# Kernel tuning notes

Hardware: AMD Instinct MI355X
Metric: run time of the kernel (lower is better)

The kernel has to match this reference:

```python
import jax, jax.numpy as jnp
import numpy as np

B, T, C = 2, 2048, 1024
NH, NKV, HD = 16, 4, 64   # n_head, n_kv_head, head_dim
WIN_LEFT = 1024           # flash-attn window_size=(1024, 0), causal


def rmsnorm(x):
    # F.rms_norm with no weight: x / sqrt(mean(x^2) + eps), eps = dtype eps
    eps = jnp.finfo(x.dtype).eps
    return x * jax.lax.rsqrt(jnp.mean(x * x, axis=-1, keepdims=True) + eps)


def rope(x, cos, sin):
    # x: [B,T,H,D]; cos/sin: [T,1,D/2] broadcast over batch and heads
    d = x.shape[-1] // 2
    x1, x2 = x[..., :d], x[..., d:]
    return jnp.concatenate([x1 * cos + x2 * sin, -x1 * sin + x2 * cos], axis=-1)


def setup_inputs() -> dict:
    key = jax.random.key(0)
    ks = jax.random.split(key, 9)
    return {
        "x":  jax.random.normal(ks[0], (B, T, C), jnp.float32),
        "x0": jax.random.normal(ks[1], (B, T, C), jnp.float32),
        "ve": jax.random.normal(ks[2], (B, T, NKV, HD), jnp.float32),
        "cos": jax.random.normal(ks[3], (T, 1, HD // 2), jnp.float32),
        "sin": jax.random.normal(ks[4], (T, 1, HD // 2), jnp.float32),
        "Wq": jax.random.normal(ks[5], (NH * HD, C), jnp.float32) * 0.02,
        "Wk": jax.random.normal(ks[6], (NKV * HD, C), jnp.float32) * 0.02,
        "Wv": jax.random.normal(ks[7], (NKV * HD, C), jnp.float32) * 0.02,
        "Wo": jax.random.normal(ks[8], (C, C), jnp.float32) * 0.02,
    }


def reference(x, x0, ve, cos, sin, Wq, Wk, Wv, Wo):
    b, t, c = x.shape
    q = (x @ Wq.T).reshape(b, t, NH, HD)
    k = (x @ Wk.T).reshape(b, t, NKV, HD)
    v = (x @ Wv.T).reshape(b, t, NKV, HD)
    v_init = v
    # is_late branch: halve_value, add_init_qkv, add_init_v all active
    v = 0.5 * v
    x0n = rmsnorm(x0)
    q = 0.5 * q + 0.5 * (x0n @ Wq.T).reshape(b, t, NH, HD)
    k = 0.5 * k + 0.5 * (x0n @ Wk.T).reshape(b, t, NKV, HD)
    v = v + 0.5 * (x0n @ Wv.T).reshape(b, t, NKV, HD)
    v = v + 0.5 * ve
    # rotary -> rms-norm -> scale 1.2 on q and k
    q = rmsnorm(rope(q, cos, sin)) * 1.2
    k = rmsnorm(rope(k, cos, sin)) * 1.2
    # GQA: repeat kv heads to match query heads
    g = NH // NKV
    k = jnp.repeat(k, g, axis=2)
    v = jnp.repeat(v, g, axis=2)
    scores = jnp.einsum("bqhd,bkhd->bhqk", q, k) / np.float32(np.sqrt(HD))
    i = jnp.arange(t)[:, None]
    j = jnp.arange(t)[None, :]
    mask = (j <= i) & (i - j <= WIN_LEFT)  # causal sliding window
    scores = jnp.where(mask, scores, jnp.finfo(scores.dtype).min)
    att = jax.nn.softmax(scores, axis=-1)
    y = jnp.einsum("bhqk,bkhd->bqhd", att, v).reshape(b, t, c)
    y = y @ Wo.T
    return (y, v_init)
```

## Files before the change

### kernel.cpp

```cpp
#include <hip/hip_runtime.h>


typedef __attribute__((ext_vector_type(8))) short bf16x8;
typedef __attribute__((ext_vector_type(4))) float f32x4;
typedef __attribute__((ext_vector_type(16))) float f32x16;
typedef unsigned short u16;
typedef unsigned int u32;

#define B_ 2
#define T_ 2048
#define C_ 1024
#define NH_ 16
#define NKV_ 4
#define WIN_ 1024
#define M_ (B_*T_)
#define EPS_ 1.1920929e-07f

__device__ __forceinline__ u16 f2bf(float f) {
  u32 u = __float_as_uint(f);
  u32 r = (u + 0x7fffu + ((u >> 16) & 1u)) >> 16;
  return (u16)r;
}
__device__ __forceinline__ float bf2f(u16 h) { return __uint_as_float(((u32)h) << 16); }

__device__ __forceinline__ void gload16(const u16* g, u16* l) {
  __builtin_amdgcn_global_load_lds((const __attribute__((address_space(1))) u32*)g,
                                   (__attribute__((address_space(3))) u32*)l, 16, 0, 0);
}
#define SWZ(row, kg) ((((row)) << 7) + ((((kg) ^ ((row) & 7))) << 4))
#define SWO(lane) (8 * (((lane) & 7) ^ (((lane) >> 3) & 7)))

__global__ __launch_bounds__(256) void k_convert_all(const float* __restrict__ Wq,
                                                     const float* __restrict__ Wk,
                                                     const float* __restrict__ Wv,
                                                     const float* __restrict__ Wo,
                                                     u16* __restrict__ dst) {
  int i4 = blockIdx.x * 256 + threadIdx.x;
  const float* src; int s0;
  if (i4 < 262144)      { src = Wq; s0 = 0; }
  else if (i4 < 327680) { src = Wk; s0 = 262144; }
  else if (i4 < 393216) { src = Wv; s0 = 327680; }
  else                  { src = Wo; s0 = 393216; }
  float4 v = ((const float4*)src)[i4 - s0];
  ushort4 o;
  o.x = f2bf(v.x); o.y = f2bf(v.y); o.z = f2bf(v.z); o.w = f2bf(v.w);
  ((ushort4*)dst)[i4] = o;
}

__global__ __launch_bounds__(256) void k_rms_combine(const float* __restrict__ x,
                                                     const float* __restrict__ x0,
                                                     u16* __restrict__ xbf,
                                                     u16* __restrict__ xmbf) {
  int row = blockIdx.x;
  int tid = threadIdx.x, lane = tid & 63, w = tid >> 6;
  const float4* px0 = (const float4*)(x0 + (size_t)row * C_);
  const float4* px  = (const float4*)(x  + (size_t)row * C_);
  float4 v0 = px0[tid];
  float ss = v0.x * v0.x + v0.y * v0.y + v0.z * v0.z + v0.w * v0.w;
  #pragma unroll
  for (int m = 1; m < 64; m <<= 1) ss += __shfl_xor(ss, m, 64);
  __shared__ float red[4];
  if (lane == 0) red[w] = ss;
  __syncthreads();
  float tot = red[0] + red[1] + red[2] + red[3];
  float rn = rsqrtf(tot * (1.0f / C_) + EPS_);
  float4 vx = px[tid];
  ushort4 om, ox;
  om.x = f2bf(0.5f * (vx.x + v0.x * rn));
  om.y = f2bf(0.5f * (vx.y + v0.y * rn));
  om.z = f2bf(0.5f * (vx.z + v0.z * rn));
  om.w = f2bf(0.5f * (vx.w + v0.w * rn));
  ox.x = f2bf(vx.x); ox.y = f2bf(vx.y); ox.z = f2bf(vx.z); ox.w = f2bf(vx.w);
  ((ushort4*)(xmbf + (size_t)row * C_))[tid] = om;
  ((ushort4*)(xbf  + (size_t)row * C_))[tid] = ox;
}

__device__ __forceinline__ void gemm_core(const u16* pa0, const u16* pb0,
                                          u16* Asl, u16* Bsl,
                                          int lane, int w, int r0, int c0,
                                          f32x4 acc[4][2]) {
  #pragma unroll
  for (int c = 0; c < 4; c++) gload16(pa0 + (size_t)c * 32 * 1024, Asl + (c * 32 + w * 8) * 64);
  #pragma unroll
  for (int c = 0; c < 2; c++) gload16(pb0 + (size_t)c * 32 * 1024, Bsl + (c * 32 + w * 8) * 64);
  int cur = 0;
  for (int kt = 0; kt < 1024; kt += 64) {
    __syncthreads();
    if (kt + 64 < 1024) {
      int nxt = cur ^ 1;
      #pragma unroll
      for (int c = 0; c < 4; c++)
        gload16(pa0 + (size_t)c * 32 * 1024 + kt + 64, Asl + nxt * 8192 + (c * 32 + w * 8) * 64);
      #pragma unroll
      for (int c = 0; c < 2; c++)
        gload16(pb0 + (size_t)c * 32 * 1024 + kt + 64, Bsl + nxt * 4096 + (c * 32 + w * 8) * 64);
    }
    const char* Ab = (const char*)(Asl + cur * 8192);
    const char* Bb = (const char*)(Bsl + cur * 4096);
    bf16x8 af[2][4], bfr[2][2];
    #pragma unroll
    for (int ks = 0; ks < 2; ks++) {
      #pragma unroll
      for (int fi = 0; fi < 4; fi++)
        af[ks][fi] = *(const bf16x8*)(Ab + SWZ(r0 + fi * 16 + (lane & 15), ks * 4 + (lane >> 4)));
      #pragma unroll
      for (int fj = 0; fj < 2; fj++)
        bfr[ks][fj] = *(const bf16x8*)(Bb + SWZ(c0 + fj * 16 + (lane & 15), ks * 4 + (lane >> 4)));
    }
    #pragma unroll
    for (int ks = 0; ks < 2; ks++)
      #pragma unroll
      for (int fi = 0; fi < 4; fi++)
        #pragma unroll
        for (int fj = 0; fj < 2; fj++)
          acc[fi][fj] = __builtin_amdgcn_mfma_f32_16x16x32_bf16(af[ks][fi], bfr[ks][fj], acc[fi][fj], 0, 0, 0);
    cur ^= 1;
  }
}

__global__ __launch_bounds__(256) void k_gemm_qkv(const u16* __restrict__ xm,
                                                  const u16* __restrict__ xb,
                                                  const u16* __restrict__ Wq,
                                                  const u16* __restrict__ Wk,
                                                  const u16* __restrict__ Wv,
                                                  u16* __restrict__ qpre,
                                                  u16* __restrict__ kpre,
                                                  u16* __restrict__ vmid,
                                                  float* __restrict__ vinit) {
  __shared__ u16 Asl[2 * 8192];
  __shared__ u16 Bsl[2 * 4096];
  int tid = threadIdx.x, lane = tid & 63, w = tid >> 6;
  int m0 = blockIdx.x * 128, bn = blockIdx.y, n0 = bn * 64;
  const u16* A; const u16* Wseg; int nseg;
  if (bn < 16)      { A = xm; Wseg = Wq; nseg = n0; }
  else if (bn < 20) { A = xm; Wseg = Wk; nseg = n0 - 1024; }
  else if (bn < 24) { A = xm; Wseg = Wv; nseg = n0 - 1280; }
  else              { A = xb; Wseg = Wv; nseg = n0 - 1536; }
  int swo = SWO(lane);
  const u16* pa0 = A    + (size_t)(m0 + w * 8 + (lane >> 3)) * 1024 + swo;
  const u16* pb0 = Wseg + (size_t)(nseg + w * 8 + (lane >> 3)) * 1024 + swo;
  int r0 = (w >> 1) * 64, c0 = (w & 1) * 32;
  f32x4 acc[4][2] = {};
  gemm_core(pa0, pb0, Asl, Bsl, lane, w, r0, c0, acc);
  #pragma unroll
  for (int fi = 0; fi < 4; fi++)
    #pragma unroll
    for (int fj = 0; fj < 2; fj++)
      #pragma unroll
      for (int i = 0; i < 4; i++) {
        int m = m0 + r0 + fi * 16 + (lane >> 4) * 4 + i;
        int nl = nseg + c0 + fj * 16 + (lane & 15);
        float v = acc[fi][fj][i];
        if (bn < 16)      qpre[(size_t)m * 1024 + nl] = f2bf(v);
        else if (bn < 20) kpre[(size_t)m * 256 + nl] = f2bf(v);
        else if (bn < 24) vmid[(size_t)m * 256 + nl] = f2bf(v);
        else              vinit[(size_t)m * 256 + nl] = v;
      }
}

__global__ __launch_bounds__(256) void k_gemm_o(const u16* __restrict__ A,
                                                const u16* __restrict__ W,
                                                float* __restrict__ y) {
  __shared__ u16 Asl[2 * 8192];
  __shared__ u16 Bsl[2 * 4096];
  int tid = threadIdx.x, lane = tid & 63, w = tid >> 6;
  int m0 = blockIdx.x * 128, n0 = blockIdx.y * 64;
  int swo = SWO(lane);
  const u16* pa0 = A + (size_t)(m0 + w * 8 + (lane >> 3)) * 1024 + swo;
  const u16* pb0 = W + (size_t)(n0 + w * 8 + (lane >> 3)) * 1024 + swo;
  int r0 = (w >> 1) * 64, c0 = (w & 1) * 32;
  f32x4 acc[4][2] = {};
  gemm_core(pa0, pb0, Asl, Bsl, lane, w, r0, c0, acc);
  #pragma unroll
  for (int fi = 0; fi < 4; fi++)
    #pragma unroll
    for (int fj = 0; fj < 2; fj++)
      #pragma unroll
      for (int i = 0; i < 4; i++) {
        int m = m0 + r0 + fi * 16 + (lane >> 4) * 4 + i;
        int n = n0 + c0 + fj * 16 + (lane & 15);
        y[(size_t)m * 1024 + n] = acc[fi][fj][i];
      }
}

__global__ __launch_bounds__(256) void k_qk_post(const u16* __restrict__ qpre,
                                                 const u16* __restrict__ kpre,
                                                 const float* __restrict__ cosp,
                                                 const float* __restrict__ sinp,
                                                 u16* __restrict__ Qh,
                                                 u16* __restrict__ Kh) {
  int w = threadIdx.x >> 6, lane = threadIdx.x & 63;
  int vid = blockIdx.x * 4 + w;
  const int NQ = B_ * T_ * NH_;
  int t; float val; size_t dst; u16* out; float scale;
  if (vid < NQ) {
    int h = vid & 15; t = (vid >> 4) & 2047; int b = vid >> 15;
    val = bf2f(qpre[(size_t)vid * 64 + lane]);
    dst = (((size_t)(b * NH_ + h) * T_) + t) * 64 + lane;
    out = Qh; scale = 0.15f;
  } else {
    int kid = vid - NQ;
    int hk = kid & 3; t = (kid >> 2) & 2047; int b = kid >> 13;
    val = bf2f(kpre[(size_t)kid * 64 + lane]);
    dst = (((size_t)(b * NKV_ + hk) * T_) + t) * 64 + lane;
    out = Kh; scale = 1.2f;
  }
  int di = lane & 31;
  float partner = __shfl_xor(val, 32, 64);
  float c = cosp[t * 32 + di], s = sinp[t * 32 + di];
  float r = (lane < 32) ? (val * c + partner * s) : (val * c - partner * s);
  float ss = r * r;
  #pragma unroll
  for (int m2 = 1; m2 < 64; m2 <<= 1) ss += __shfl_xor(ss, m2, 64);
  r *= rsqrtf(ss * (1.0f / 64.0f) + EPS_) * scale;
  out[dst] = f2bf(r);
}

__global__ __launch_bounds__(256) void k_vt(const u16* __restrict__ vmid,
                                            const float* __restrict__ ve,
                                            u16* __restrict__ VtG) {
  __shared__ u16 S[64][72];
  int tid = threadIdx.x;
  int t0 = blockIdx.x * 64, hk = blockIdx.y, b = blockIdx.z;
  {
    int tl = tid >> 2, dg = (tid & 3) * 16;
    const int4* pvm = (const int4*)(vmid + (size_t)(b * T_ + t0 + tl) * 256 + hk * 64 + dg);
    const float4* pve = (const float4*)(ve + ((size_t)(b * T_ + t0 + tl) * 4 + hk) * 64 + dg);
    int4 vv[2]; vv[0] = pvm[0]; vv[1] = pvm[1];
    const u16* vm = (const u16*)vv;
    float4 vf[4]; vf[0] = pve[0]; vf[1] = pve[1]; vf[2] = pve[2]; vf[3] = pve[3];
    const float* vfp = (const float*)vf;
    u16 r[16];
    #pragma unroll
    for (int e = 0; e < 16; e++) r[e] = f2bf(bf2f(vm[e]) + 0.5f * vfp[e]);
    *(int4*)&S[tl][dg] = *(int4*)&r[0];
    *(int4*)&S[tl][dg + 8] = *(int4*)&r[8];
  }
  __syncthreads();
  {
    int dl = tid >> 2, tg = (tid & 3) * 16;
    u16 r[16];
    #pragma unroll
    for (int j = 0; j < 16; j++) r[j] = S[tg + j][dl];
    u16* o = VtG + ((size_t)((b * NKV_ + hk) * 64 + dl)) * T_ + t0 + tg;
    *(int4*)&o[0] = *(int4*)&r[0];
    *(int4*)&o[8] = *(int4*)&r[8];
  }
}

__global__ __launch_bounds__(512) void k_attn(const u16* __restrict__ Qh,
                                              const u16* __restrict__ Kh,
                                              const u16* __restrict__ VtG,
                                              u16* __restrict__ ao) {
  __shared__ u16 Ksl[2][64 * 64];
  __shared__ u16 Vsl[2][64 * 64];
  __shared__ float Sc[8][32];
  int tid = threadIdx.x, lane = tid & 63, w = tid >> 6;
  int hi = lane >> 5, qc = lane & 31;
  int qt = blockIdx.x, h = blockIdx.y, b = blockIdx.z;
  int hk = h >> 2;
  int q0 = qt * 256, wq0 = q0 + w * 32;
  const u16* Qp = Qh + ((size_t)(b * NH_ + h) * T_) * 64;
  const u16* Kp = Kh + ((size_t)(b * NKV_ + hk) * T_) * 64;
  int swo = SWO(lane);
  const u16* pk0 = Kp + (size_t)(w * 8 + (lane >> 3)) * 64 + swo;
  const u16* pv0 = VtG + ((size_t)((b * NKV_ + hk) * 64 + w * 8 + (lane >> 3))) * T_ + swo;

  bf16x8 qf[4];
  #pragma unroll
  for (int ds = 0; ds < 4; ds++)
    qf[ds] = *(const bf16x8*)(Qp + (size_t)(wq0 + qc) * 64 + ds * 16 + hi * 8);

  f32x16 o0 = {}, o1 = {};
  float mrun = -1e4f, lrun = 0.f;
  int kt_lo = q0 - WIN_; if (kt_lo < 0) kt_lo = 0;
  int kt_hi = q0 + 192;

  gload16(pk0 + (size_t)kt_lo * 64, &Ksl[0][w * 512]);
  gload16(pv0 + kt_lo,              &Vsl[0][w * 512]);
  int cur = 0;
  for (int kt = kt_lo; kt <= kt_hi; kt += 64) {
    __syncthreads();
    if (kt + 64 <= kt_hi) {
      gload16(pk0 + (size_t)(kt + 64) * 64, &Ksl[cur ^ 1][w * 512]);
      gload16(pv0 + kt + 64,                &Vsl[cur ^ 1][w * 512]);
    }
    if (kt <= wq0 + 31 && kt + 63 >= wq0 - WIN_) {
      const char* Kb = (const char*)&Ksl[cur][0];
      const char* Vb = (const char*)&Vsl[cur][0];
      f32x16 st[2] = {};
      #pragma unroll
      for (int kt2 = 0; kt2 < 2; kt2++)
        #pragma unroll
        for (int ds = 0; ds < 4; ds++) {
          bf16x8 kf = *(const bf16x8*)(Kb + SWZ(kt2 * 32 + qc, 2 * ds + hi));
          st[kt2] = __builtin_amdgcn_mfma_f32_32x32x16_bf16(kf, qf[ds], st[kt2], 0, 0, 0);
        }
      bool full = (kt + 63 <= wq0) && (wq0 + 31 - kt <= WIN_);
      int D0 = wq0 + qc - kt;
      float p[2][16];
      float tmax = -1e30f;
      #pragma unroll
      for (int kt2 = 0; kt2 < 2; kt2++)
        #pragma unroll
        for (int r = 0; r < 16; r++) {
          float sv = st[kt2][r];
          if (!full) {
            int jl = 32 * kt2 + (r & 3) + 8 * (r >> 2) + 4 * hi;
            sv = (jl <= D0 && jl >= D0 - WIN_) ? sv : -1e9f;
          }
          p[kt2][r] = sv;
          tmax = fmaxf(tmax, sv);
        }
      tmax = fmaxf(tmax, __shfl_xor(tmax, 32, 64));
      if (__any(tmax > mrun + 8.0f)) {
        float mnew = fmaxf(mrun, tmax);
        float alpha = __expf(mrun - mnew);
        mrun = mnew; lrun *= alpha;
        if (hi == 0) Sc[w][qc] = alpha;
        #pragma unroll
        for (int r = 0; r < 16; r++) {
          float al = Sc[w][(r & 3) + 8 * (r >> 2) + 4 * hi];
          o0[r] *= al; o1[r] *= al;
        }
      }
      float rsum = 0.f;
      u32 pw[2][8];
      #pragma unroll
      for (int kt2 = 0; kt2 < 2; kt2++)
        #pragma unroll
        for (int c = 0; c < 8; c++) {
          float pe = __expf(p[kt2][2 * c] - mrun);
          float po = __expf(p[kt2][2 * c + 1] - mrun);
          rsum += pe + po;
          pw[kt2][c] = __builtin_amdgcn_perm(__float_as_uint(po), __float_as_uint(pe), 0x07060302u);
        }
      rsum += __shfl_xor(rsum, 32, 64);
      lrun += rsum;
      #pragma unroll
      for (int kt2 = 0; kt2 < 2; kt2++)
        #pragma unroll
        for (int ksp = 0; ksp < 2; ksp++) {
          union { u32 uw[4]; bf16x8 v; } U;
          #pragma unroll
          for (int c = 0; c < 2; c++) {
            u32 x = pw[kt2][4 * ksp + c];
            u32 y = pw[kt2][4 * ksp + 2 + c];
            u32 xs = (u32)__shfl_xor((int)x, 32, 64);
            u32 ys = (u32)__shfl_xor((int)y, 32, 64);
            U.uw[c]     = hi ? ys : x;
            U.uw[2 + c] = hi ? y : xs;
          }
          int ks = 2 * kt2 + ksp;
          bf16x8 v0 = *(const bf16x8*)(Vb + SWZ(qc,      2 * ks + hi));
          bf16x8 v1 = *(const bf16x8*)(Vb + SWZ(32 + qc, 2 * ks + hi));
          o0 = __builtin_amdgcn_mfma_f32_32x32x16_bf16(U.v, v0, o0, 0, 0, 0);
          o1 = __builtin_amdgcn_mfma_f32_32x32x16_bf16(U.v, v1, o1, 0, 0, 0);
        }
    }
    cur ^= 1;
  }
  if (hi == 0) Sc[w][qc] = 1.0f / lrun;
  #pragma unroll
  for (int r = 0; r < 16; r++) {
    int q = (r & 3) + 8 * (r >> 2) + 4 * hi;
    float il = Sc[w][q];
    size_t base = ((size_t)(b * T_ + wq0 + q) * NH_ + h) * 64;
    ao[base + qc]      = f2bf(o0[r] * il);
    ao[base + 32 + qc] = f2bf(o1[r] * il);
  }
}

extern "C" void kernel_launch(void* const* d_in, const int* in_sizes, int n_in,
                              void* d_out, int out_size, void* d_ws, size_t ws_size,
                              hipStream_t stream) {
  const float* x    = (const float*)d_in[0];
  const float* x0   = (const float*)d_in[1];
  const float* ve   = (const float*)d_in[2];
  const float* cosp = (const float*)d_in[3];
  const float* sinp = (const float*)d_in[4];
  const float* Wq   = (const float*)d_in[5];
  const float* Wk   = (const float*)d_in[6];
  const float* Wv   = (const float*)d_in[7];
  const float* Wo   = (const float*)d_in[8];
  float* out = (float*)d_out;

  u16* ws = (u16*)d_ws;
  size_t off = 0;
  u16* xbf  = ws + off; off += (size_t)M_ * C_;
  u16* xmbf = ws + off; off += (size_t)M_ * C_;
  u16* Wqb  = ws + off; off += (size_t)1024 * 1024;
  u16* Wkb  = ws + off; off += (size_t)256 * 1024;
  u16* Wvb  = ws + off; off += (size_t)256 * 1024;
  u16* Wob  = ws + off; off += (size_t)1024 * 1024;
  u16* qpre = ws + off; off += (size_t)M_ * 1024;
  u16* kpre = ws + off; off += (size_t)M_ * 256;
  u16* vmid = ws + off; off += (size_t)M_ * 256;
  u16* VtG  = ws + off; off += (size_t)B_ * NKV_ * 64 * T_;
  u16* aob = xbf;
  u16* Qhb = xmbf;
  u16* Khb = Wqb;

  k_convert_all<<<2560, 256, 0, stream>>>(Wq, Wk, Wv, Wo, Wqb);
  k_rms_combine<<<4096, 256, 0, stream>>>(x, x0, xbf, xmbf);
  k_gemm_qkv<<<dim3(32, 28), 256, 0, stream>>>(xmbf, xbf, Wqb, Wkb, Wvb,
                                               qpre, kpre, vmid, out + (size_t)M_ * C_);
  k_qk_post<<<20480, 256, 0, stream>>>(qpre, kpre, cosp, sinp, Qhb, Khb);
  k_vt<<<dim3(32, 4, 2), 256, 0, stream>>>(vmid, ve, VtG);
  k_attn<<<dim3(8, 16, 2), 512, 0, stream>>>(Qhb, Khb, VtG, aob);
  k_gemm_o<<<dim3(32, 16), 256, 0, stream>>>(aob, Wob, out);
}
```

Measured before the change: 214.2 us.

## Rewrite attention as split-KV two-wave blocks and enlarge GEMM tiles to 128x128

The attention kernel now gives each 128-thread block one 32-query tile and splits the key range between two waves. Each wave streams K/V fragments straight from global memory into registers instead of staging them in shared memory, and the two partial softmax states are merged at the end through shared memory. Blocks are ordered with the heaviest query tiles first and grouped by KV head for cache reuse. The GEMMs switch to 128x128 tiles with 4x4 MFMA accumulators per wave, but drop the double-buffered LDS prefetch for a single buffer with two barriers per k-step. This trades load latency hiding for more reuse per tile.

```diff
diff --git a/kernel.cpp b/kernel.cpp
--- a/kernel.cpp
+++ b/kernel.cpp
@@ -78,43 +78,32 @@
 __device__ __forceinline__ void gemm_core(const u16* pa0, const u16* pb0,
                                           u16* Asl, u16* Bsl,
                                           int lane, int w, int r0, int c0,
-                                          f32x4 acc[4][2]) {
-  #pragma unroll
-  for (int c = 0; c < 4; c++) gload16(pa0 + (size_t)c * 32 * 1024, Asl + (c * 32 + w * 8) * 64);
-  #pragma unroll
-  for (int c = 0; c < 2; c++) gload16(pb0 + (size_t)c * 32 * 1024, Bsl + (c * 32 + w * 8) * 64);
-  int cur = 0;
+                                          f32x4 acc[4][4]) {
+  const char* Ab = (const char*)Asl;
+  const char* Bb = (const char*)Bsl;
   for (int kt = 0; kt < 1024; kt += 64) {
     __syncthreads();
-    if (kt + 64 < 1024) {
-      int nxt = cur ^ 1;
-      #pragma unroll
-      for (int c = 0; c < 4; c++)
-        gload16(pa0 + (size_t)c * 32 * 1024 + kt + 64, Asl + nxt * 8192 + (c * 32 + w * 8) * 64);
-      #pragma unroll
-      for (int c = 0; c < 2; c++)
-        gload16(pb0 + (size_t)c * 32 * 1024 + kt + 64, Bsl + nxt * 4096 + (c * 32 + w * 8) * 64);
-    }
-    const char* Ab = (const char*)(Asl + cur * 8192);
-    const char* Bb = (const char*)(Bsl + cur * 4096);
-    bf16x8 af[2][4], bfr[2][2];
-    #pragma unroll
-    for (int ks = 0; ks < 2; ks++) {
-      #pragma unroll
-      for (int fi = 0; fi < 4; fi++)
-        af[ks][fi] = *(const bf16x8*)(Ab + SWZ(r0 + fi * 16 + (lane & 15), ks * 4 + (lane >> 4)));
-      #pragma unroll
-      for (int fj = 0; fj < 2; fj++)
-        bfr[ks][fj] = *(const bf16x8*)(Bb + SWZ(c0 + fj * 16 + (lane & 15), ks * 4 + (lane >> 4)));
-    }
+    #pragma unroll
+    for (int c = 0; c < 4; c++) {
+      gload16(pa0 + (size_t)c * 32 * 1024 + kt, Asl + (c * 32 + w * 8) * 64);
+      gload16(pb0 + (size_t)c * 32 * 1024 + kt, Bsl + (c * 32 + w * 8) * 64);
+    }
+    __syncthreads();
+    bf16x8 af[2][4], bfr[2][4];
+    #pragma unroll
+    for (int ks = 0; ks < 2; ks++)
+      #pragma unroll
+      for (int fi = 0; fi < 4; fi++) {
+        af[ks][fi]  = *(const bf16x8*)(Ab + SWZ(r0 + fi * 16 + (lane & 15), ks * 4 + (lane >> 4)));
+        bfr[ks][fi] = *(const bf16x8*)(Bb + SWZ(c0 + fi * 16 + (lane & 15), ks * 4 + (lane >> 4)));
+      }
     #pragma unroll
     for (int ks = 0; ks < 2; ks++)
       #pragma unroll
       for (int fi = 0; fi < 4; fi++)
         #pragma unroll
-        for (int fj = 0; fj < 2; fj++)
+        for (int fj = 0; fj < 4; fj++)
           acc[fi][fj] = __builtin_amdgcn_mfma_f32_16x16x32_bf16(af[ks][fi], bfr[ks][fj], acc[fi][fj], 0, 0, 0);
-    cur ^= 1;
   }
 }
 
@@ -127,59 +116,59 @@
                                                   u16* __restrict__ kpre,
                                                   u16* __restrict__ vmid,
                                                   float* __restrict__ vinit) {
-  __shared__ u16 Asl[2 * 8192];
-  __shared__ u16 Bsl[2 * 4096];
+  __shared__ u16 Asl[128 * 64];
+  __shared__ u16 Bsl[128 * 64];
   int tid = threadIdx.x, lane = tid & 63, w = tid >> 6;
-  int m0 = blockIdx.x * 128, bn = blockIdx.y, n0 = bn * 64;
+  int m0 = blockIdx.x * 128, bn = blockIdx.y, n0 = bn * 128;
   const u16* A; const u16* Wseg; int nseg;
-  if (bn < 16)      { A = xm; Wseg = Wq; nseg = n0; }
-  else if (bn < 20) { A = xm; Wseg = Wk; nseg = n0 - 1024; }
-  else if (bn < 24) { A = xm; Wseg = Wv; nseg = n0 - 1280; }
+  if (bn < 8)       { A = xm; Wseg = Wq; nseg = n0; }
+  else if (bn < 10) { A = xm; Wseg = Wk; nseg = n0 - 1024; }
+  else if (bn < 12) { A = xm; Wseg = Wv; nseg = n0 - 1280; }
   else              { A = xb; Wseg = Wv; nseg = n0 - 1536; }
   int swo = SWO(lane);
   const u16* pa0 = A    + (size_t)(m0 + w * 8 + (lane >> 3)) * 1024 + swo;
   const u16* pb0 = Wseg + (size_t)(nseg + w * 8 + (lane >> 3)) * 1024 + swo;
-  int r0 = (w >> 1) * 64, c0 = (w & 1) * 32;
-  f32x4 acc[4][2] = {};
+  int r0 = (w & 1) * 64, c0 = (w >> 1) * 64;
+  f32x4 acc[4][4] = {};
   gemm_core(pa0, pb0, Asl, Bsl, lane, w, r0, c0, acc);
   #pragma unroll
   for (int fi = 0; fi < 4; fi++)
     #pragma unroll
-    for (int fj = 0; fj < 2; fj++)
+    for (int fj = 0; fj < 4; fj++)
       #pragma unroll
       for (int i = 0; i < 4; i++) {
-        int m = m0 + r0 + fi * 16 + (lane >> 4) * 4 + i;
+        int mrow = m0 + r0 + fi * 16 + (lane >> 4) * 4 + i;
         int nl = nseg + c0 + fj * 16 + (lane & 15);
         float v = acc[fi][fj][i];
-        if (bn < 16)      qpre[(size_t)m * 1024 + nl] = f2bf(v);
-        else if (bn < 20) kpre[(size_t)m * 256 + nl] = f2bf(v);
-        else if (bn < 24) vmid[(size_t)m * 256 + nl] = f2bf(v);
-        else              vinit[(size_t)m * 256 + nl] = v;
+        if (bn < 8)       qpre[(size_t)mrow * 1024 + nl] = f2bf(v);
+        else if (bn < 10) kpre[(size_t)mrow * 256 + nl] = f2bf(v);
+        else if (bn < 12) vmid[(size_t)mrow * 256 + nl] = f2bf(v);
+        else              vinit[(size_t)mrow * 256 + nl] = v;
       }
 }
 
 __global__ __launch_bounds__(256) void k_gemm_o(const u16* __restrict__ A,
                                                 const u16* __restrict__ W,
                                                 float* __restrict__ y) {
-  __shared__ u16 Asl[2 * 8192];
-  __shared__ u16 Bsl[2 * 4096];
+  __shared__ u16 Asl[128 * 64];
+  __shared__ u16 Bsl[128 * 64];
   int tid = threadIdx.x, lane = tid & 63, w = tid >> 6;
-  int m0 = blockIdx.x * 128, n0 = blockIdx.y * 64;
+  int m0 = blockIdx.x * 128, n0 = blockIdx.y * 128;
   int swo = SWO(lane);
   const u16* pa0 = A + (size_t)(m0 + w * 8 + (lane >> 3)) * 1024 + swo;
   const u16* pb0 = W + (size_t)(n0 + w * 8 + (lane >> 3)) * 1024 + swo;
-  int r0 = (w >> 1) * 64, c0 = (w & 1) * 32;
-  f32x4 acc[4][2] = {};
+  int r0 = (w & 1) * 64, c0 = (w >> 1) * 64;
+  f32x4 acc[4][4] = {};
   gemm_core(pa0, pb0, Asl, Bsl, lane, w, r0, c0, acc);
   #pragma unroll
   for (int fi = 0; fi < 4; fi++)
     #pragma unroll
-    for (int fj = 0; fj < 2; fj++)
+    for (int fj = 0; fj < 4; fj++)
       #pragma unroll
       for (int i = 0; i < 4; i++) {
-        int m = m0 + r0 + fi * 16 + (lane >> 4) * 4 + i;
+        int mrow = m0 + r0 + fi * 16 + (lane >> 4) * 4 + i;
         int n = n0 + c0 + fj * 16 + (lane & 15);
-        y[(size_t)m * 1024 + n] = acc[fi][fj][i];
+        y[(size_t)mrow * 1024 + n] = acc[fi][fj][i];
       }
 }
 
@@ -248,126 +237,164 @@
   }
 }
 
-__global__ __launch_bounds__(512) void k_attn(const u16* __restrict__ Qh,
-                                              const u16* __restrict__ Kh,
-                                              const u16* __restrict__ VtG,
-                                              u16* __restrict__ ao) {
-  __shared__ u16 Ksl[2][64 * 64];
-  __shared__ u16 Vsl[2][64 * 64];
-  __shared__ float Sc[8][32];
-  int tid = threadIdx.x, lane = tid & 63, w = tid >> 6;
+__global__ __launch_bounds__(128, 4) void k_attn(const u16* __restrict__ Qh,
+                                                 const u16* __restrict__ Kh,
+                                                 const u16* __restrict__ VtG,
+                                                 u16* __restrict__ ao) {
+  __shared__ float OS[64][17];
+  __shared__ float Ml[2][32], Ll[2][32], Sc[2][32];
+  int tid = threadIdx.x, lane = tid & 63, wv = tid >> 6;
   int hi = lane >> 5, qc = lane & 31;
-  int qt = blockIdx.x, h = blockIdx.y, b = blockIdx.z;
-  int hk = h >> 2;
-  int q0 = qt * 256, wq0 = q0 + w * 32;
-  const u16* Qp = Qh + ((size_t)(b * NH_ + h) * T_) * 64;
+  int bid = blockIdx.x;
+  int g = bid & 7, within = bid >> 3;
+  int b = g >> 2, hk = g & 3;
+  int hq = within >> 6, qt = 63 - (within & 63);
+  int h = hk * 4 + hq;
+  int q0w = qt * 32;
+  const u16* Qp = Qh + ((size_t)(b * NH_ + h) * T_ + q0w) * 64;
   const u16* Kp = Kh + ((size_t)(b * NKV_ + hk) * T_) * 64;
-  int swo = SWO(lane);
-  const u16* pk0 = Kp + (size_t)(w * 8 + (lane >> 3)) * 64 + swo;
-  const u16* pv0 = VtG + ((size_t)((b * NKV_ + hk) * 64 + w * 8 + (lane >> 3))) * T_ + swo;
-
-  bf16x8 qf[4];
-  #pragma unroll
-  for (int ds = 0; ds < 4; ds++)
-    qf[ds] = *(const bf16x8*)(Qp + (size_t)(wq0 + qc) * 64 + ds * 16 + hi * 8);
+  const u16* Vp = VtG + ((size_t)(b * NKV_ + hk) * 64) * T_;
+
+  bf16x8 qf0 = *(const bf16x8*)(Qp + (size_t)qc * 64 + 0  + hi * 8);
+  bf16x8 qf1 = *(const bf16x8*)(Qp + (size_t)qc * 64 + 16 + hi * 8);
+  bf16x8 qf2 = *(const bf16x8*)(Qp + (size_t)qc * 64 + 32 + hi * 8);
+  bf16x8 qf3 = *(const bf16x8*)(Qp + (size_t)qc * 64 + 48 + hi * 8);
 
   f32x16 o0 = {}, o1 = {};
-  float mrun = -1e4f, lrun = 0.f;
-  int kt_lo = q0 - WIN_; if (kt_lo < 0) kt_lo = 0;
-  int kt_hi = q0 + 192;
-
-  gload16(pk0 + (size_t)kt_lo * 64, &Ksl[0][w * 512]);
-  gload16(pv0 + kt_lo,              &Vsl[0][w * 512]);
-  int cur = 0;
-  for (int kt = kt_lo; kt <= kt_hi; kt += 64) {
-    __syncthreads();
-    if (kt + 64 <= kt_hi) {
-      gload16(pk0 + (size_t)(kt + 64) * 64, &Ksl[cur ^ 1][w * 512]);
-      gload16(pv0 + kt + 64,                &Vsl[cur ^ 1][w * 512]);
-    }
-    if (kt <= wq0 + 31 && kt + 63 >= wq0 - WIN_) {
-      const char* Kb = (const char*)&Ksl[cur][0];
-      const char* Vb = (const char*)&Vsl[cur][0];
-      f32x16 st[2] = {};
-      #pragma unroll
-      for (int kt2 = 0; kt2 < 2; kt2++)
-        #pragma unroll
-        for (int ds = 0; ds < 4; ds++) {
-          bf16x8 kf = *(const bf16x8*)(Kb + SWZ(kt2 * 32 + qc, 2 * ds + hi));
-          st[kt2] = __builtin_amdgcn_mfma_f32_32x32x16_bf16(kf, qf[ds], st[kt2], 0, 0, 0);
-        }
-      bool full = (kt + 63 <= wq0) && (wq0 + 31 - kt <= WIN_);
-      int D0 = wq0 + qc - kt;
-      float p[2][16];
-      float tmax = -1e30f;
-      #pragma unroll
-      for (int kt2 = 0; kt2 < 2; kt2++)
-        #pragma unroll
-        for (int r = 0; r < 16; r++) {
-          float sv = st[kt2][r];
-          if (!full) {
-            int jl = 32 * kt2 + (r & 3) + 8 * (r >> 2) + 4 * hi;
-            sv = (jl <= D0 && jl >= D0 - WIN_) ? sv : -1e9f;
-          }
-          p[kt2][r] = sv;
-          tmax = fmaxf(tmax, sv);
-        }
-      tmax = fmaxf(tmax, __shfl_xor(tmax, 32, 64));
-      if (__any(tmax > mrun + 8.0f)) {
-        float mnew = fmaxf(mrun, tmax);
-        float alpha = __expf(mrun - mnew);
-        mrun = mnew; lrun *= alpha;
-        if (hi == 0) Sc[w][qc] = alpha;
-        #pragma unroll
-        for (int r = 0; r < 16; r++) {
-          float al = Sc[w][(r & 3) + 8 * (r >> 2) + 4 * hi];
-          o0[r] *= al; o1[r] *= al;
-        }
-      }
-      float rsum = 0.f;
-      u32 pw[2][8];
-      #pragma unroll
-      for (int kt2 = 0; kt2 < 2; kt2++)
-        #pragma unroll
-        for (int c = 0; c < 8; c++) {
-          float pe = __expf(p[kt2][2 * c] - mrun);
-          float po = __expf(p[kt2][2 * c + 1] - mrun);
-          rsum += pe + po;
-          pw[kt2][c] = __builtin_amdgcn_perm(__float_as_uint(po), __float_as_uint(pe), 0x07060302u);
-        }
-      rsum += __shfl_xor(rsum, 32, 64);
-      lrun += rsum;
-      #pragma unroll
-      for (int kt2 = 0; kt2 < 2; kt2++)
-        #pragma unroll
-        for (int ksp = 0; ksp < 2; ksp++) {
-          union { u32 uw[4]; bf16x8 v; } U;
-          #pragma unroll
-          for (int c = 0; c < 2; c++) {
-            u32 x = pw[kt2][4 * ksp + c];
-            u32 y = pw[kt2][4 * ksp + 2 + c];
-            u32 xs = (u32)__shfl_xor((int)x, 32, 64);
-            u32 ys = (u32)__shfl_xor((int)y, 32, 64);
-            U.uw[c]     = hi ? ys : x;
-            U.uw[2 + c] = hi ? y : xs;
-          }
-          int ks = 2 * kt2 + ksp;
-          bf16x8 v0 = *(const bf16x8*)(Vb + SWZ(qc,      2 * ks + hi));
-          bf16x8 v1 = *(const bf16x8*)(Vb + SWZ(32 + qc, 2 * ks + hi));
-          o0 = __builtin_amdgcn_mfma_f32_32x32x16_bf16(U.v, v0, o0, 0, 0, 0);
-          o1 = __builtin_amdgcn_mfma_f32_32x32x16_bf16(U.v, v1, o1, 0, 0, 0);
-        }
-    }
-    cur ^= 1;
-  }
-  if (hi == 0) Sc[w][qc] = 1.0f / lrun;
+  float m = -1e4f, l = 0.f;
+  int klo = q0w - WIN_; if (klo < 0) klo = 0;
+  int kt0 = klo + wv * 32;
+
+  bf16x8 kf0, kf1, kf2, kf3, vf0, vf1, vf2, vf3;
+  if (kt0 <= q0w) {
+    const u16* kp = Kp + (size_t)(kt0 + qc) * 64 + hi * 8;
+    kf0 = *(const bf16x8*)(kp + 0);  kf1 = *(const bf16x8*)(kp + 16);
+    kf2 = *(const bf16x8*)(kp + 32); kf3 = *(const bf16x8*)(kp + 48);
+    const u16* vp = Vp + (size_t)qc * T_ + kt0 + hi * 8;
+    vf0 = *(const bf16x8*)(vp + 0);  vf1 = *(const bf16x8*)(vp + 16);
+    vf2 = *(const bf16x8*)(vp + 32 * T_);  vf3 = *(const bf16x8*)(vp + 32 * T_ + 16);
+  }
+
+  for (int kt = kt0; kt <= q0w; kt += 64) {
+    f32x16 st = {};
+    __builtin_amdgcn_s_setprio(1);
+    st = __builtin_amdgcn_mfma_f32_32x32x16_bf16(kf0, qf0, st, 0, 0, 0);
+    st = __builtin_amdgcn_mfma_f32_32x32x16_bf16(kf1, qf1, st, 0, 0, 0);
+    st = __builtin_amdgcn_mfma_f32_32x32x16_bf16(kf2, qf2, st, 0, 0, 0);
+    st = __builtin_amdgcn_mfma_f32_32x32x16_bf16(kf3, qf3, st, 0, 0, 0);
+    __builtin_amdgcn_s_setprio(0);
+    int ktn = kt + 64;
+    bool more = (ktn <= q0w);
+    if (more) {
+      const u16* kp = Kp + (size_t)(ktn + qc) * 64 + hi * 8;
+      kf0 = *(const bf16x8*)(kp + 0);  kf1 = *(const bf16x8*)(kp + 16);
+      kf2 = *(const bf16x8*)(kp + 32); kf3 = *(const bf16x8*)(kp + 48);
+    }
+    bool full = (kt != q0w) && (kt != q0w - WIN_);
+    float p[16];
+    float tmax = -1e30f;
+    int iq = q0w + qc;
+    #pragma unroll
+    for (int r = 0; r < 16; r++) {
+      float sv = st[r];
+      if (!full) {
+        int j = kt + (r & 3) + 8 * (r >> 2) + 4 * hi;
+        sv = (j <= iq && iq - j <= WIN_) ? sv : -1e9f;
+      }
+      p[r] = sv;
+      tmax = fmaxf(tmax, sv);
+    }
+    tmax = fmaxf(tmax, __shfl_xor(tmax, 32, 64));
+    if (__any(tmax > m + 8.0f)) {
+      float mn = fmaxf(m, tmax);
+      float al = __expf(m - mn);
+      m = mn; l *= al;
+      if (hi == 0) Sc[wv][qc] = al;
+      #pragma unroll
+      for (int r = 0; r < 16; r++) {
+        float a2 = Sc[wv][(r & 3) + 8 * (r >> 2) + 4 * hi];
+        o0[r] *= a2; o1[r] *= a2;
+      }
+    }
+    float rsum = 0.f;
+    u32 pw[8];
+    #pragma unroll
+    for (int c = 0; c < 8; c++) {
+      float pe = __expf(p[2 * c] - m);
+      float po = __expf(p[2 * c + 1] - m);
+      rsum += pe + po;
+      pw[c] = __builtin_amdgcn_perm(__float_as_uint(po), __float_as_uint(pe), 0x07060302u);
+    }
+    rsum += __shfl_xor(rsum, 32, 64);
+    l += rsum;
+    __builtin_amdgcn_s_setprio(1);
+    #pragma unroll
+    for (int ksp = 0; ksp < 2; ksp++) {
+      union { u32 uw[4]; bf16x8 v; } U;
+      #pragma unroll
+      for (int c = 0; c < 2; c++) {
+        u32 x = pw[4 * ksp + c];
+        u32 y = pw[4 * ksp + 2 + c];
+        u32 xs = (u32)__shfl_xor((int)x, 32, 64);
+        u32 ys = (u32)__shfl_xor((int)y, 32, 64);
+        U.uw[c]     = hi ? ys : x;
+        U.uw[2 + c] = hi ? y : xs;
+      }
+      if (ksp == 0) {
+        o0 = __builtin_amdgcn_mfma_f32_32x32x16_bf16(U.v, vf0, o0, 0, 0, 0);
+        o1 = __builtin_amdgcn_mfma_f32_32x32x16_bf16(U.v, vf2, o1, 0, 0, 0);
+      } else {
+        o0 = __builtin_amdgcn_mfma_f32_32x32x16_bf16(U.v, vf1, o0, 0, 0, 0);
+        o1 = __builtin_amdgcn_mfma_f32_32x32x16_bf16(U.v, vf3, o1, 0, 0, 0);
+      }
+    }
+    __builtin_amdgcn_s_setprio(0);
+    if (more) {
+      const u16* vp = Vp + (size_t)qc * T_ + ktn + hi * 8;
+      vf0 = *(const bf16x8*)(vp + 0);  vf1 = *(const bf16x8*)(vp + 16);
+      vf2 = *(const bf16x8*)(vp + 32 * T_);  vf3 = *(const bf16x8*)(vp + 32 * T_ + 16);
+    }
+  }
+
+  if (hi == 0) { Ml[wv][qc] = m; Ll[wv][qc] = l; }
+  __syncthreads();
+  float sfac[16];
   #pragma unroll
   for (int r = 0; r < 16; r++) {
     int q = (r & 3) + 8 * (r >> 2) + 4 * hi;
-    float il = Sc[w][q];
-    size_t base = ((size_t)(b * T_ + wq0 + q) * NH_ + h) * 64;
-    ao[base + qc]      = f2bf(o0[r] * il);
-    ao[base + 32 + qc] = f2bf(o1[r] * il);
+    float m0v = Ml[0][q], m1v = Ml[1][q];
+    float l0v = Ll[0][q], l1v = Ll[1][q];
+    float ms = fmaxf(m0v, m1v);
+    float s0 = __expf(m0v - ms), s1 = __expf(m1v - ms);
+    float inv = 1.0f / (l0v * s0 + l1v * s1);
+    sfac[r] = (wv == 0 ? s0 : s1) * inv;
+  }
+  if (wv == 1) {
+    #pragma unroll
+    for (int r = 0; r < 16; r++) OS[lane][r] = o0[r] * sfac[r];
+  }
+  __syncthreads();
+  if (wv == 0) {
+    #pragma unroll
+    for (int r = 0; r < 16; r++) {
+      int q = (r & 3) + 8 * (r >> 2) + 4 * hi;
+      size_t base = ((size_t)(b * T_ + q0w + q) * NH_ + h) * 64;
+      ao[base + qc] = f2bf(o0[r] * sfac[r] + OS[lane][r]);
+    }
+  }
+  __syncthreads();
+  if (wv == 1) {
+    #pragma unroll
+    for (int r = 0; r < 16; r++) OS[lane][r] = o1[r] * sfac[r];
+  }
+  __syncthreads();
+  if (wv == 0) {
+    #pragma unroll
+    for (int r = 0; r < 16; r++) {
+      int q = (r & 3) + 8 * (r >> 2) + 4 * hi;
+      size_t base = ((size_t)(b * T_ + q0w + q) * NH_ + h) * 64;
+      ao[base + 32 + qc] = f2bf(o1[r] * sfac[r] + OS[lane][r]);
+    }
   }
 }
 
@@ -403,10 +430,10 @@
 
   k_convert_all<<<2560, 256, 0, stream>>>(Wq, Wk, Wv, Wo, Wqb);
   k_rms_combine<<<4096, 256, 0, stream>>>(x, x0, xbf, xmbf);
-  k_gemm_qkv<<<dim3(32, 28), 256, 0, stream>>>(xmbf, xbf, Wqb, Wkb, Wvb,
+  k_gemm_qkv<<<dim3(32, 14), 256, 0, stream>>>(xmbf, xbf, Wqb, Wkb, Wvb,
                                                qpre, kpre, vmid, out + (size_t)M_ * C_);
   k_qk_post<<<20480, 256, 0, stream>>>(qpre, kpre, cosp, sinp, Qhb, Khb);
   k_vt<<<dim3(32, 4, 2), 256, 0, stream>>>(vmid, ve, VtG);
-  k_attn<<<dim3(8, 16, 2), 512, 0, stream>>>(Qhb, Khb, VtG, aob);
-  k_gemm_o<<<dim3(32, 16), 256, 0, stream>>>(aob, Wob, out);
-}
+  k_attn<<<2048, 128, 0, stream>>>(Qhb, Khb, VtG, aob);
+  k_gemm_o<<<dim3(32, 8), 256, 0, stream>>>(aob, Wob, out);
+}
```

Measured after the change: 260.2 us. 21.5% more time.
